# Kernel optimization log

Hardware: AMD Instinct MI355X
Metric: run time of the kernel (lower is better)

Reference implementation:

```python
import jax, jax.numpy as jnp
import numpy as np

N_ENT = 100000   # n_entities
N_HE = 20000     # n_hyperedges
D = 128          # in_dim == out_dim
NNZ_A = 3200000  # nnz of A_in (avg degree 32)
NNZ_H = 1000000  # nnz of each hyperedge incidence matrix


def spmm(rows, cols, vals, x, n_rows):
    """COO sparse (n_rows, n_cols) @ dense x (n_cols, d) -> (n_rows, d)."""
    return jax.ops.segment_sum(vals[:, None] * x[cols], rows, num_segments=n_rows)


def setup_inputs() -> dict:
    key = jax.random.key(0)
    ks = jax.random.split(key, 20)
    ri = lambda k, n, hi: jax.random.randint(k, (n,), 0, hi, dtype=jnp.int32)
    rv = lambda k, n: jax.random.uniform(k, (n,), dtype=jnp.float32) * 0.1
    inp = {
        "ego": jax.random.normal(ks[0], (N_ENT, D), dtype=jnp.float32),
        "A_rows": ri(ks[1], NNZ_A, N_ENT),
        "A_cols": ri(ks[2], NNZ_A, N_ENT),
        "A_vals": rv(ks[3], NNZ_A),
        "p1_rows": ri(ks[4], NNZ_H, N_HE),
        "p1_cols": ri(ks[5], NNZ_H, N_ENT),
        "p1_vals": rv(ks[6], NNZ_H),
        "p2_rows": ri(ks[7], NNZ_H, N_ENT),
        "p2_cols": ri(ks[8], NNZ_H, N_HE),
        "p2_vals": rv(ks[9], NNZ_H),
        "l1_rows": ri(ks[10], NNZ_H, N_HE),
        "l1_cols": ri(ks[11], NNZ_H, N_ENT),
        "l1_vals": rv(ks[12], NNZ_H),
        "l2_rows": ri(ks[13], NNZ_H, N_ENT),
        "l2_cols": ri(ks[14], NNZ_H, N_HE),
        "l2_vals": rv(ks[15], NNZ_H),
        "W1": jax.random.normal(ks[16], (D, D), dtype=jnp.float32) * (1.0 / np.sqrt(D)),
        "b1": jnp.zeros((D,), dtype=jnp.float32),
        "W2": jax.random.normal(ks[17], (D, D), dtype=jnp.float32) * (1.0 / np.sqrt(D)),
        "b2": jnp.zeros((D,), dtype=jnp.float32),
    }
    return inp


def reference(ego, A_rows, A_cols, A_vals,
              p1_rows, p1_cols, p1_vals, p2_rows, p2_cols, p2_vals,
              l1_rows, l1_cols, l1_vals, l2_rows, l2_cols, l2_vals,
              W1, b1, W2, b2):
    # side = A_in @ ego
    side = spmm(A_rows, A_cols, A_vals, ego, N_ENT)
    # proj = norm_proj2 @ (norm_proj1 @ ego)
    proj = spmm(p2_rows, p2_cols, p2_vals,
                spmm(p1_rows, p1_cols, p1_vals, ego, N_HE), N_ENT)
    # lib = norm_lib2 @ (norm_lib1 @ ego)
    lib = spmm(l2_rows, l2_cols, l2_vals,
               spmm(l1_rows, l1_cols, l1_vals, ego, N_HE), N_ENT)
    side = side + proj + lib
    # bi-interaction: LeakyReLU(Linear(ego+side)) + LeakyReLU(Linear(ego*side))
    sum_emb = jax.nn.leaky_relu((ego + side) @ W1.T + b1, negative_slope=0.01)
    bi_emb = jax.nn.leaky_relu((ego * side) @ W2.T + b2, negative_slope=0.01)
    # attention=True -> sum of both branches; message_dropout is identity in eval
    return sum_emb + bi_emb
```

## Files before the change

### kernel.cpp

```cpp
#include <hip/hip_runtime.h>

#define DIM 128
#define N_ENT 100000
#define N_HE  20000
#define NFE 3125
#define NFH 625
#define NFINE 4375
#define CAPF 2000
#define NCC 49
#define CAPC 110000
#define CHB 27
#define TA 4096
#define RPA 16
#define RPT 8

typedef __attribute__((ext_vector_type(8))) _Float16 f16x8;
typedef __attribute__((ext_vector_type(4))) _Float16 f16x4;
typedef __attribute__((ext_vector_type(4))) float f32x4;

__device__ __forceinline__ unsigned bf16_rne(float x) {
  unsigned b = __float_as_uint(x);
  return (b + 0x7fffu + ((b >> 16) & 1u)) >> 16;
}
__device__ __forceinline__ unsigned pack2(float lo, float hi) {
  return bf16_rne(lo) | (bf16_rne(hi) << 16);
}
__device__ __forceinline__ float bf16lo(unsigned u) { return __uint_as_float(u << 16); }
__device__ __forceinline__ float bf16hi(unsigned u) { return __uint_as_float(u & 0xffff0000u); }

__global__ __launch_bounds__(256) void cvt_bf16_kernel(const float* __restrict__ src,
                                                       unsigned* __restrict__ dst,
                                                       int n4) {
  for (int i = blockIdx.x * 256 + threadIdx.x; i < n4; i += gridDim.x * 256) {
    float4 v = reinterpret_cast<const float4*>(src)[i];
    reinterpret_cast<uint2*>(dst)[i] = make_uint2(pack2(v.x, v.y), pack2(v.z, v.w));
  }
}

__global__ __launch_bounds__(256) void cvt_w_kernel(const float* __restrict__ w1,
                                                    const float* __restrict__ w2,
                                                    _Float16* __restrict__ w1h,
                                                    _Float16* __restrict__ w2h) {
  const int half = blockIdx.x >= 8;
  const float* src = half ? w2 : w1;
  _Float16* dst = half ? w2h : w1h;
  const int b = half ? (int)blockIdx.x - 8 : (int)blockIdx.x;
  const int n4 = DIM * DIM / 4;
  for (int i = b * 256 + threadIdx.x; i < n4; i += 8 * 256) {
    float4 v = reinterpret_cast<const float4*>(src)[i];
    f16x4 o;
    o.x = (_Float16)v.x; o.y = (_Float16)v.y; o.z = (_Float16)v.z; o.w = (_Float16)v.w;
    *reinterpret_cast<f16x4*>(dst + (size_t)i * 4) = o;
  }
}

struct SegB {
  const int* rows[5];
  const int* cols[5];
  const float* vals[5];
  int nnz[5];
  int blk_pfx[6];
};

__device__ __forceinline__ int seg_of(const int* pfx, int b) {
  int s = 0;
  while (s < 4 && b >= pfx[s + 1]) s++;
  return s;
}

__global__ __launch_bounds__(256) void binA_kernel(SegB a, int2* __restrict__ heapC,
                                                   int2* __restrict__ heapF,
                                                   int* __restrict__ gcurC,
                                                   int* __restrict__ gcurF) {
  __shared__ int2 srec[TA];
  __shared__ int s_cnt[NFH];
  __shared__ int s_delta[NFH];
  __shared__ int s_part[256];
  const int t = threadIdx.x;
  const int s = seg_of(a.blk_pfx, (int)blockIdx.x);
  const bool ent = (s < 3);
  const unsigned cbase = (s == 1) ? 100000u : ((s == 2) ? 120000u : 0u);
  const int heBase = (s == 3) ? NFE : (NFE + NFH);
  const int nbins = ent ? NCC : NFH;
  const int base = (blockIdx.x - a.blk_pfx[s]) * TA;
  const int cnt_here = min(TA, a.nnz[s] - base);
  const int* __restrict__ rows = a.rows[s];
  const int* __restrict__ cols = a.cols[s];
  const float* __restrict__ vals = a.vals[s];

  for (int i = t; i < nbins; i += 256) s_cnt[i] = 0;
  __syncthreads();

  uint2 rec[RPA];
#pragma unroll
  for (int j = 0; j < RPA; j++) {
    int li = t + j * 256;
    if (li < cnt_here) {
      int e = base + li;
      int r = rows[e];
      unsigned vb = bf16_rne(vals[e]);
      if (ent) {
        unsigned ccol = (unsigned)cols[e] + cbase;
        rec[j].x = (unsigned)(r & 31) | (ccol << 6) | ((unsigned)((r >> 5) & 63) << 24);
        rec[j].y = (vb << 16) | (unsigned)(r >> 11);
        atomicAdd(&s_cnt[r >> 11], 1);
      } else {
        rec[j].x = (unsigned)(r & 31) | ((unsigned)cols[e] << 6);
        rec[j].y = (vb << 16) | (unsigned)(r >> 5);
        atomicAdd(&s_cnt[r >> 5], 1);
      }
    }
  }
  __syncthreads();

  {
    const int chunk = (nbins + 255) / 256;
    const int lo = min(t * chunk, nbins);
    const int hi = min(lo + chunk, nbins);
    int sum = 0;
    for (int i = lo; i < hi; i++) sum += s_cnt[i];
    s_part[t] = sum;
    __syncthreads();
    for (int off = 1; off < 256; off <<= 1) {
      int v = (t >= off) ? s_part[t - off] : 0;
      __syncthreads();
      s_part[t] += v;
      __syncthreads();
    }
    int run = t ? s_part[t - 1] : 0;
    for (int i = lo; i < hi; i++) { int v = s_cnt[i]; s_cnt[i] = run; run += v; }
  }
  __syncthreads();

  for (int i = t; i < nbins; i += 256) {
    int st = s_cnt[i];
    int en = (i == nbins - 1) ? cnt_here : s_cnt[i + 1];
    int c = en - st;
    if (c > 0) {
      if (ent) {
        int gb = atomicAdd(&gcurC[i], c);
        s_delta[i] = i * CAPC + gb - st;
      } else {
        int fg = heBase + i;
        int gb = atomicAdd(&gcurF[fg], c);
        s_delta[i] = fg * CAPF + gb - st;
      }
    }
  }
  __syncthreads();

#pragma unroll
  for (int j = 0; j < RPA; j++) {
    int li = t + j * 256;
    if (li < cnt_here) {
      int bin = ent ? (int)(rec[j].y & 63u) : (int)(rec[j].y & 0x3FFu);
      int p = atomicAdd(&s_cnt[bin], 1);
      srec[p] = make_int2((int)rec[j].x, (int)rec[j].y);
    }
  }
  __syncthreads();

  int2* __restrict__ heap = ent ? heapC : heapF;
  for (int i = t; i < cnt_here; i += 256) {
    int2 rr = srec[i];
    unsigned ry = (unsigned)rr.y;
    int bin = ent ? (int)(ry & 63u) : (int)(ry & 0x3FFu);
    int addr = s_delta[bin] + i;
    int rel = ent ? (addr - bin * CAPC) : (addr - (heBase + bin) * CAPF);
    int cap = ent ? CAPC : CAPF;
    if (rel < cap) heap[addr] = make_int2(rr.x, (int)(ry & 0xFFFF0000u));
  }
}

__global__ __launch_bounds__(256) void binB_kernel(const int2* __restrict__ heapC,
                                                   const int* __restrict__ gcurC,
                                                   int2* __restrict__ heapF,
                                                   int* __restrict__ gcurF) {
  __shared__ int2 srec[TA];
  __shared__ int s_cnt[64];
  __shared__ int s_delta[64];
  const int t = threadIdx.x;
  const int c = blockIdx.x / CHB;
  const int ch = blockIdx.x % CHB;
  const int ccnt = min(gcurC[c], CAPC);
  const int base = ch * TA;
  const int cnt_here = min(TA, ccnt - base);
  if (cnt_here <= 0) return;
  const int2* __restrict__ src = heapC + (size_t)c * CAPC + base;

  if (t < 64) s_cnt[t] = 0;
  __syncthreads();

  uint2 rec[RPA];
#pragma unroll
  for (int j = 0; j < RPA; j++) {
    int li = t + j * 256;
    if (li < cnt_here) {
      int2 v = src[li];
      rec[j] = make_uint2((unsigned)v.x, (unsigned)v.y);
      atomicAdd(&s_cnt[(rec[j].x >> 24) & 63u], 1);
    }
  }
  __syncthreads();

  if (t == 0) {
    int run = 0;
    for (int i = 0; i < 64; i++) { int v = s_cnt[i]; s_cnt[i] = run; run += v; }
  }
  __syncthreads();

  if (t < 64) {
    int st = s_cnt[t];
    int en = (t == 63) ? cnt_here : s_cnt[t + 1];
    int cc = en - st;
    if (cc > 0) {
      int fine = c * 64 + t;
      int gb = atomicAdd(&gcurF[fine], cc);
      s_delta[t] = fine * CAPF + gb - st;
    }
  }
  __syncthreads();

#pragma unroll
  for (int j = 0; j < RPA; j++) {
    int li = t + j * 256;
    if (li < cnt_here) {
      int bin = (int)((rec[j].x >> 24) & 63u);
      int p = atomicAdd(&s_cnt[bin], 1);
      srec[p] = make_int2((int)rec[j].x, (int)rec[j].y);
    }
  }
  __syncthreads();

  for (int i = t; i < cnt_here; i += 256) {
    int2 rr = srec[i];
    int bin = (int)(((unsigned)rr.x >> 24) & 63u);
    int addr = s_delta[bin] + i;
    int rel = addr - (c * 64 + bin) * CAPF;
    if (rel < CAPF)
      heapF[addr] = make_int2((int)((unsigned)rr.x & 0x00FFFFFFu), rr.y);
  }
}

__device__ __forceinline__ void bf16_fma4(float4& acc, uint2 g, float v) {
  acc.x = fmaf(v, __uint_as_float(g.x << 16), acc.x);
  acc.y = fmaf(v, __uint_as_float(g.x & 0xffff0000u), acc.y);
  acc.z = fmaf(v, __uint_as_float(g.y << 16), acc.z);
  acc.w = fmaf(v, __uint_as_float(g.y & 0xffff0000u), acc.w);
}

__device__ __forceinline__ float lrelu(float v) { return v > 0.0f ? v : 0.01f * v; }

template <bool BF16SIDE>
__global__ __launch_bounds__(256, 8) void spmm_ent_kernel(
    const int2* __restrict__ heapF, const int* __restrict__ gcurF,
    const unsigned* __restrict__ xall, float* __restrict__ outf,
    unsigned* __restrict__ sideh) {
  __shared__ int2 srec[CAPF];
  __shared__ int sh_cnt[32];
  __shared__ int sh_off[33];
  __shared__ int sh_cur[32];
  const int b = blockIdx.x;
  const int t = threadIdx.x;
  const int cnt = min(gcurF[b], CAPF);
  const size_t base = (size_t)b * CAPF;

  if (t < 32) sh_cnt[t] = 0;
  __syncthreads();

  int2 rec[RPT];
#pragma unroll
  for (int j = 0; j < RPT; j++) {
    int idx = t + j * 256;
    if (idx < cnt) {
      rec[j] = heapF[base + idx];
      atomicAdd(&sh_cnt[((unsigned)rec[j].x) & 31u], 1);
    }
  }
  __syncthreads();

  if (t == 0) {
    int run = 0;
    for (int i = 0; i < 32; i++) { sh_off[i] = run; sh_cur[i] = run; run += sh_cnt[i]; }
    sh_off[32] = run;
  }
  __syncthreads();

#pragma unroll
  for (int j = 0; j < RPT; j++) {
    int idx = t + j * 256;
    if (idx < cnt) {
      int rl = (int)(((unsigned)rec[j].x) & 31u);
      int p = atomicAdd(&sh_cur[rl], 1);
      srec[p] = rec[j];
    }
  }
  __syncthreads();

  const int grp = t >> 5, sub = t & 31;
  const unsigned* __restrict__ xs = xall + sub * 2;
  const int row0 = b * 32;
#pragma unroll
  for (int i = 0; i < 4; i++) {
    const int r = grp + i * 8;
    float4 acc = make_float4(0.f, 0.f, 0.f, 0.f);
    const int je = sh_off[r + 1];
    int j = sh_off[r];
    for (; j + 8 <= je; j += 8) {
      int2 r0 = srec[j], r1 = srec[j + 1], r2 = srec[j + 2], r3 = srec[j + 3];
      int2 r4 = srec[j + 4], r5 = srec[j + 5], r6 = srec[j + 6], r7 = srec[j + 7];
      uint2 g0 = *reinterpret_cast<const uint2*>(xs + (((unsigned)r0.x) & 0x00FFFFC0u));
      uint2 g1 = *reinterpret_cast<const uint2*>(xs + (((unsigned)r1.x) & 0x00FFFFC0u));
      uint2 g2 = *reinterpret_cast<const uint2*>(xs + (((unsigned)r2.x) & 0x00FFFFC0u));
      uint2 g3 = *reinterpret_cast<const uint2*>(xs + (((unsigned)r3.x) & 0x00FFFFC0u));
      uint2 g4 = *reinterpret_cast<const uint2*>(xs + (((unsigned)r4.x) & 0x00FFFFC0u));
      uint2 g5 = *reinterpret_cast<const uint2*>(xs + (((unsigned)r5.x) & 0x00FFFFC0u));
      uint2 g6 = *reinterpret_cast<const uint2*>(xs + (((unsigned)r6.x) & 0x00FFFFC0u));
      uint2 g7 = *reinterpret_cast<const uint2*>(xs + (((unsigned)r7.x) & 0x00FFFFC0u));
      bf16_fma4(acc, g0, __int_as_float(r0.y));
      bf16_fma4(acc, g1, __int_as_float(r1.y));
      bf16_fma4(acc, g2, __int_as_float(r2.y));
      bf16_fma4(acc, g3, __int_as_float(r3.y));
      bf16_fma4(acc, g4, __int_as_float(r4.y));
      bf16_fma4(acc, g5, __int_as_float(r5.y));
      bf16_fma4(acc, g6, __int_as_float(r6.y));
      bf16_fma4(acc, g7, __int_as_float(r7.y));
    }
    for (; j + 2 <= je; j += 2) {
      int2 r0 = srec[j], r1 = srec[j + 1];
      uint2 g0 = *reinterpret_cast<const uint2*>(xs + (((unsigned)r0.x) & 0x00FFFFC0u));
      uint2 g1 = *reinterpret_cast<const uint2*>(xs + (((unsigned)r1.x) & 0x00FFFFC0u));
      bf16_fma4(acc, g0, __int_as_float(r0.y));
      bf16_fma4(acc, g1, __int_as_float(r1.y));
    }
    if (j < je) {
      int2 r0 = srec[j];
      uint2 g0 = *reinterpret_cast<const uint2*>(xs + (((unsigned)r0.x) & 0x00FFFFC0u));
      bf16_fma4(acc, g0, __int_as_float(r0.y));
    }
    if (BF16SIDE) {
      *reinterpret_cast<uint2*>(sideh + (size_t)(row0 + r) * 64 + sub * 2) =
          make_uint2(pack2(acc.x, acc.y), pack2(acc.z, acc.w));
    } else {
      *reinterpret_cast<float4*>(outf + (size_t)(row0 + r) * DIM + sub * 4) = acc;
    }
  }
}

__global__ __launch_bounds__(256, 8) void spmm_he_kernel(
    const int2* __restrict__ heapF, const int* __restrict__ gcurF,
    const unsigned* __restrict__ egoh,
    unsigned* __restrict__ tmp1h, unsigned* __restrict__ tmp2h) {
  __shared__ int2 srec[CAPF];
  __shared__ int sh_cnt[32];
  __shared__ int sh_off[33];
  __shared__ int sh_cur[32];
  const int half = blockIdx.x >= NFH;
  const int b = half ? (int)blockIdx.x - NFH : (int)blockIdx.x;
  const int fine = (half ? NFE + NFH : NFE) + b;
  unsigned* outh = half ? tmp2h : tmp1h;
  const int t = threadIdx.x;
  const int cnt = min(gcurF[fine], CAPF);
  const size_t base = (size_t)fine * CAPF;

  if (t < 32) sh_cnt[t] = 0;
  __syncthreads();

  int2 rec[RPT];
#pragma unroll
  for (int j = 0; j < RPT; j++) {
    int idx = t + j * 256;
    if (idx < cnt) {
      rec[j] = heapF[base + idx];
      atomicAdd(&sh_cnt[((unsigned)rec[j].x) & 31u], 1);
    }
  }
  __syncthreads();

  if (t == 0) {
    int run = 0;
    for (int i = 0; i < 32; i++) { sh_off[i] = run; sh_cur[i] = run; run += sh_cnt[i]; }
    sh_off[32] = run;
  }
  __syncthreads();

#pragma unroll
  for (int j = 0; j < RPT; j++) {
    int idx = t + j * 256;
    if (idx < cnt) {
      int rl = (int)(((unsigned)rec[j].x) & 31u);
      int p = atomicAdd(&sh_cur[rl], 1);
      srec[p] = rec[j];
    }
  }
  __syncthreads();

  const int grp = t >> 5, sub = t & 31;
  const unsigned* __restrict__ xs = egoh + sub * 2;
  const int row0 = b * 32;
#pragma unroll
  for (int i = 0; i < 4; i++) {
    const int r = grp + i * 8;
    float4 acc = make_float4(0.f, 0.f, 0.f, 0.f);
    const int je = sh_off[r + 1];
    int j = sh_off[r];
    for (; j + 8 <= je; j += 8) {
      int2 r0 = srec[j], r1 = srec[j + 1], r2 = srec[j + 2], r3 = srec[j + 3];
      int2 r4 = srec[j + 4], r5 = srec[j + 5], r6 = srec[j + 6], r7 = srec[j + 7];
      uint2 g0 = *reinterpret_cast<const uint2*>(xs + (((unsigned)r0.x) & 0x00FFFFC0u));
      uint2 g1 = *reinterpret_cast<const uint2*>(xs + (((unsigned)r1.x) & 0x00FFFFC0u));
      uint2 g2 = *reinterpret_cast<const uint2*>(xs + (((unsigned)r2.x) & 0x00FFFFC0u));
      uint2 g3 = *reinterpret_cast<const uint2*>(xs + (((unsigned)r3.x) & 0x00FFFFC0u));
      uint2 g4 = *reinterpret_cast<const uint2*>(xs + (((unsigned)r4.x) & 0x00FFFFC0u));
      uint2 g5 = *reinterpret_cast<const uint2*>(xs + (((unsigned)r5.x) & 0x00FFFFC0u));
      uint2 g6 = *reinterpret_cast<const uint2*>(xs + (((unsigned)r6.x) & 0x00FFFFC0u));
      uint2 g7 = *reinterpret_cast<const uint2*>(xs + (((unsigned)r7.x) & 0x00FFFFC0u));
      bf16_fma4(acc, g0, __int_as_float(r0.y));
      bf16_fma4(acc, g1, __int_as_float(r1.y));
      bf16_fma4(acc, g2, __int_as_float(r2.y));
      bf16_fma4(acc, g3, __int_as_float(r3.y));
      bf16_fma4(acc, g4, __int_as_float(r4.y));
      bf16_fma4(acc, g5, __int_as_float(r5.y));
      bf16_fma4(acc, g6, __int_as_float(r6.y));
      bf16_fma4(acc, g7, __int_as_float(r7.y));
    }
    for (; j + 2 <= je; j += 2) {
      int2 r0 = srec[j], r1 = srec[j + 1];
      uint2 g0 = *reinterpret_cast<const uint2*>(xs + (((unsigned)r0.x) & 0x00FFFFC0u));
      uint2 g1 = *reinterpret_cast<const uint2*>(xs + (((unsigned)r1.x) & 0x00FFFFC0u));
      bf16_fma4(acc, g0, __int_as_float(r0.y));
      bf16_fma4(acc, g1, __int_as_float(r1.y));
    }
    if (j < je) {
      int2 r0 = srec[j];
      uint2 g0 = *reinterpret_cast<const uint2*>(xs + (((unsigned)r0.x) & 0x00FFFFC0u));
      bf16_fma4(acc, g0, __int_as_float(r0.y));
    }
    *reinterpret_cast<uint2*>(outh + (size_t)(row0 + r) * 64 + sub * 2) =
        make_uint2(pack2(acc.x, acc.y), pack2(acc.z, acc.w));
  }
}

template <bool BF16SIDE>
__global__ __launch_bounds__(256, 3) void mfma_epilogue_kernel(
    const float* __restrict__ ego,
    const unsigned* __restrict__ sideh,
    float* __restrict__ out,
    const _Float16* __restrict__ w1h,
    const _Float16* __restrict__ w2h,
    const float* __restrict__ b1,
    const float* __restrict__ b2) {
  __shared__ __align__(16) _Float16 s_sum[64 * DIM];
  __shared__ __align__(16) _Float16 s_prod[64 * DIM];
  const int t = threadIdx.x;
  const int row0 = blockIdx.x * 64;

  for (int i = t; i < 64 * (DIM / 4); i += 256) {
    int r = i >> 5;
    int c4 = (i & 31) * 4;
    int gr = row0 + r;
    float4 e4 = make_float4(0.f, 0.f, 0.f, 0.f);
    float sx = 0.f, sy = 0.f, sz = 0.f, sw = 0.f;
    if (gr < N_ENT) {
      e4 = *reinterpret_cast<const float4*>(ego + (size_t)gr * DIM + c4);
      if (BF16SIDE) {
        uint2 s2 = *reinterpret_cast<const uint2*>(sideh + (size_t)gr * 64 + (c4 >> 1));
        sx = bf16lo(s2.x); sy = bf16hi(s2.x); sz = bf16lo(s2.y); sw = bf16hi(s2.y);
      } else {
        float4 sd4 = *reinterpret_cast<const float4*>(out + (size_t)gr * DIM + c4);
        sx = sd4.x; sy = sd4.y; sz = sd4.z; sw = sd4.w;
      }
    }
    int sidx = (r * DIM + c4) ^ ((r & 7) << 3);
    f16x4 sv, pv;
    sv.x = (_Float16)(e4.x + sx);
    sv.y = (_Float16)(e4.y + sy);
    sv.z = (_Float16)(e4.z + sz);
    sv.w = (_Float16)(e4.w + sw);
    pv.x = (_Float16)(e4.x * sx);
    pv.y = (_Float16)(e4.y * sy);
    pv.z = (_Float16)(e4.z * sz);
    pv.w = (_Float16)(e4.w * sw);
    *reinterpret_cast<f16x4*>(&s_sum[sidx]) = sv;
    *reinterpret_cast<f16x4*>(&s_prod[sidx]) = pv;
  }
  __syncthreads();

  const int w = t >> 6;
  const int l = t & 63;
  const int lr = l & 15;
  const int lk = l >> 4;

  f32x4 acc1[8] = {};
  f32x4 acc2[8] = {};

#pragma unroll
  for (int ks = 0; ks < 4; ks++) {
    int arow = w * 16 + lr;
    int sidx = (arow * DIM + ks * 32 + lk * 8) ^ ((arow & 7) << 3);
    f16x8 a1 = *reinterpret_cast<const f16x8*>(&s_sum[sidx]);
    f16x8 a2 = *reinterpret_cast<const f16x8*>(&s_prod[sidx]);
#pragma unroll
    for (int jt = 0; jt < 8; jt++) {
      int fidx = (jt * 16 + lr) * DIM + ks * 32 + lk * 8;
      f16x8 bw1 = *reinterpret_cast<const f16x8*>(w1h + fidx);
      f16x8 bw2 = *reinterpret_cast<const f16x8*>(w2h + fidx);
      acc1[jt] = __builtin_amdgcn_mfma_f32_16x16x32_f16(a1, bw1, acc1[jt], 0, 0, 0);
      acc2[jt] = __builtin_amdgcn_mfma_f32_16x16x32_f16(a2, bw2, acc2[jt], 0, 0, 0);
    }
  }

#pragma unroll
  for (int jt = 0; jt < 8; jt++) {
    int col = jt * 16 + lr;
    float bb1 = b1[col];
    float bb2 = b2[col];
#pragma unroll
    for (int r = 0; r < 4; r++) {
      int gr = row0 + w * 16 + lk * 4 + r;
      if (gr < N_ENT)
        out[(size_t)gr * DIM + col] = lrelu(acc1[jt][r] + bb1) + lrelu(acc2[jt][r] + bb2);
    }
  }
}

extern "C" void kernel_launch(void* const* d_in, const int* in_sizes, int n_in,
                              void* d_out, int out_size, void* d_ws, size_t ws_size,
                              hipStream_t stream) {
  const float* ego     = (const float*)d_in[0];
  const float* W1      = (const float*)d_in[16];
  const float* b1      = (const float*)d_in[17];
  const float* W2      = (const float*)d_in[18];
  const float* b2      = (const float*)d_in[19];

  int2* heapF = (int2*)d_ws;
  int2* heapC = heapF + (size_t)NFINE * CAPF;
  int*  gcurC = (int*)(heapC + (size_t)NCC * CAPC);
  int*  gcurF = gcurC + NCC;
  unsigned* sideh = (unsigned*)(gcurF + NFINE);
  unsigned* egoh  = (unsigned*)heapC;
  unsigned* tmp1h = egoh + (size_t)N_ENT * 64;
  unsigned* tmp2h = tmp1h + (size_t)N_HE * 64;
  _Float16* w1h = (_Float16*)(tmp2h + (size_t)N_HE * 64);
  _Float16* w2h = w1h + DIM * DIM;

  const size_t need_bf16side =
      (size_t)((char*)(sideh + (size_t)N_ENT * 64) - (char*)d_ws);
  const bool bf16side = (ws_size >= need_bf16side);

  hipMemsetAsync(gcurC, 0, (size_t)(NCC + NFINE) * sizeof(int), stream);

  SegB sg;
  sg.rows[0] = (const int*)d_in[1];  sg.cols[0] = (const int*)d_in[2];  sg.vals[0] = (const float*)d_in[3];  sg.nnz[0] = in_sizes[1];
  sg.rows[1] = (const int*)d_in[7];  sg.cols[1] = (const int*)d_in[8];  sg.vals[1] = (const float*)d_in[9];  sg.nnz[1] = in_sizes[7];
  sg.rows[2] = (const int*)d_in[13]; sg.cols[2] = (const int*)d_in[14]; sg.vals[2] = (const float*)d_in[15]; sg.nnz[2] = in_sizes[13];
  sg.rows[3] = (const int*)d_in[4];  sg.cols[3] = (const int*)d_in[5];  sg.vals[3] = (const float*)d_in[6];  sg.nnz[3] = in_sizes[4];
  sg.rows[4] = (const int*)d_in[10]; sg.cols[4] = (const int*)d_in[11]; sg.vals[4] = (const float*)d_in[12]; sg.nnz[4] = in_sizes[10];
  int pfx = 0;
  for (int s = 0; s < 5; s++) {
    sg.blk_pfx[s] = pfx;
    pfx += (sg.nnz[s] + TA - 1) / TA;
  }
  sg.blk_pfx[5] = pfx;

  binA_kernel<<<dim3(pfx), dim3(256), 0, stream>>>(sg, heapC, heapF, gcurC, gcurF);
  binB_kernel<<<dim3(NCC * CHB), dim3(256), 0, stream>>>(heapC, gcurC, heapF, gcurF);

  cvt_bf16_kernel<<<dim3(2048), dim3(256), 0, stream>>>(ego, egoh, N_ENT * (DIM / 4));
  cvt_w_kernel<<<dim3(16), dim3(256), 0, stream>>>(W1, W2, w1h, w2h);

  float* out = (float*)d_out;

  spmm_he_kernel<<<dim3(2 * NFH), dim3(256), 0, stream>>>(heapF, gcurF, egoh, tmp1h, tmp2h);

  if (bf16side) {
    spmm_ent_kernel<true><<<dim3(NFE), dim3(256), 0, stream>>>(
        heapF, gcurF, egoh, out, sideh);
    mfma_epilogue_kernel<true><<<dim3((N_ENT + 63) / 64), dim3(256), 0, stream>>>(
        ego, sideh, out, w1h, w2h, b1, b2);
  } else {
    spmm_ent_kernel<false><<<dim3(NFE), dim3(256), 0, stream>>>(
        heapF, gcurF, egoh, out, sideh);
    mfma_epilogue_kernel<false><<<dim3((N_ENT + 63) / 64), dim3(256), 0, stream>>>(
        ego, sideh, out, w1h, w2h, b1, b2);
  }
}
```

Before: 430.0 us.

## Rebin rows into finer non-power-of-two groups and merge conversion kernels

Changes the row binning from power-of-two groups of 32 rows to 25 rows per entity bin and 20 rows per hyperedge bin. This adds more SpMM blocks with smaller shared-memory record buffers and capacities, aiming at better occupancy and load balance. The two conversion kernels are merged into one launch, and the epilogue's launch bounds are raised to 4 blocks per CU. Bin computation now needs integer divisions, and the smaller per-bin capacities raise the risk of silently dropped records on overflow.

```diff
diff --git a/kernel.cpp b/kernel.cpp
--- a/kernel.cpp
+++ b/kernel.cpp
@@ -3,16 +3,22 @@
 #define DIM 128
 #define N_ENT 100000
 #define N_HE  20000
-#define NFE 3125
-#define NFH 625
-#define NFINE 4375
-#define CAPF 2000
-#define NCC 49
+#define ROWS_E 25
+#define NFE2 4000
+#define CAPE 1600
+#define NCC 50
+#define NFB 80
 #define CAPC 110000
 #define CHB 27
+#define ROWS_H 20
+#define NFH2 1000
+#define CAPH2 1280
+#define HEB0 (NFE2 * CAPE)
+#define NFINE 6000
 #define TA 4096
 #define RPA 16
-#define RPT 8
+#define RPT_E 7
+#define RPT_H 5
 
 typedef __attribute__((ext_vector_type(8))) _Float16 f16x8;
 typedef __attribute__((ext_vector_type(4))) _Float16 f16x4;
@@ -28,29 +34,30 @@
 __device__ __forceinline__ float bf16lo(unsigned u) { return __uint_as_float(u << 16); }
 __device__ __forceinline__ float bf16hi(unsigned u) { return __uint_as_float(u & 0xffff0000u); }
 
-__global__ __launch_bounds__(256) void cvt_bf16_kernel(const float* __restrict__ src,
-                                                       unsigned* __restrict__ dst,
-                                                       int n4) {
-  for (int i = blockIdx.x * 256 + threadIdx.x; i < n4; i += gridDim.x * 256) {
-    float4 v = reinterpret_cast<const float4*>(src)[i];
-    reinterpret_cast<uint2*>(dst)[i] = make_uint2(pack2(v.x, v.y), pack2(v.z, v.w));
-  }
-}
-
-__global__ __launch_bounds__(256) void cvt_w_kernel(const float* __restrict__ w1,
-                                                    const float* __restrict__ w2,
-                                                    _Float16* __restrict__ w1h,
-                                                    _Float16* __restrict__ w2h) {
-  const int half = blockIdx.x >= 8;
-  const float* src = half ? w2 : w1;
-  _Float16* dst = half ? w2h : w1h;
-  const int b = half ? (int)blockIdx.x - 8 : (int)blockIdx.x;
-  const int n4 = DIM * DIM / 4;
-  for (int i = b * 256 + threadIdx.x; i < n4; i += 8 * 256) {
-    float4 v = reinterpret_cast<const float4*>(src)[i];
-    f16x4 o;
-    o.x = (_Float16)v.x; o.y = (_Float16)v.y; o.z = (_Float16)v.z; o.w = (_Float16)v.w;
-    *reinterpret_cast<f16x4*>(dst + (size_t)i * 4) = o;
+__global__ __launch_bounds__(256) void cvt_all_kernel(const float* __restrict__ ego,
+                                                      unsigned* __restrict__ egoh,
+                                                      const float* __restrict__ w1,
+                                                      const float* __restrict__ w2,
+                                                      _Float16* __restrict__ w1h,
+                                                      _Float16* __restrict__ w2h) {
+  if (blockIdx.x < 2048) {
+    const int n4 = N_ENT * (DIM / 4);
+    for (int i = blockIdx.x * 256 + threadIdx.x; i < n4; i += 2048 * 256) {
+      float4 v = reinterpret_cast<const float4*>(ego)[i];
+      reinterpret_cast<uint2*>(egoh)[i] = make_uint2(pack2(v.x, v.y), pack2(v.z, v.w));
+    }
+  } else {
+    const int half = blockIdx.x >= 2056;
+    const float* src = half ? w2 : w1;
+    _Float16* dst = half ? w2h : w1h;
+    const int b = (int)blockIdx.x - (half ? 2056 : 2048);
+    const int n4 = DIM * DIM / 4;
+    for (int i = b * 256 + threadIdx.x; i < n4; i += 8 * 256) {
+      float4 v = reinterpret_cast<const float4*>(src)[i];
+      f16x4 o;
+      o.x = (_Float16)v.x; o.y = (_Float16)v.y; o.z = (_Float16)v.z; o.w = (_Float16)v.w;
+      *reinterpret_cast<f16x4*>(dst + (size_t)i * 4) = o;
+    }
   }
 }
 
@@ -73,15 +80,16 @@
                                                    int* __restrict__ gcurC,
                                                    int* __restrict__ gcurF) {
   __shared__ int2 srec[TA];
-  __shared__ int s_cnt[NFH];
-  __shared__ int s_delta[NFH];
+  __shared__ int s_cnt[NFH2];
+  __shared__ int s_delta[NFH2];
   __shared__ int s_part[256];
   const int t = threadIdx.x;
   const int s = seg_of(a.blk_pfx, (int)blockIdx.x);
   const bool ent = (s < 3);
   const unsigned cbase = (s == 1) ? 100000u : ((s == 2) ? 120000u : 0u);
-  const int heBase = (s == 3) ? NFE : (NFE + NFH);
-  const int nbins = ent ? NCC : NFH;
+  const int heSegOff = (s == 4) ? NFH2 * CAPH2 : 0;
+  const int heCurOff = NFE2 + ((s == 4) ? NFH2 : 0);
+  const int nbins = ent ? NCC : NFH2;
   const int base = (blockIdx.x - a.blk_pfx[s]) * TA;
   const int cnt_here = min(TA, a.nnz[s] - base);
   const int* __restrict__ rows = a.rows[s];
@@ -97,17 +105,23 @@
     int li = t + j * 256;
     if (li < cnt_here) {
       int e = base + li;
-      int r = rows[e];
+      unsigned r = (unsigned)rows[e];
       unsigned vb = bf16_rne(vals[e]);
       if (ent) {
+        unsigned fine = r / ROWS_E;
+        unsigned rowlocal = r - fine * ROWS_E;
+        unsigned coarse = fine / NFB;
+        unsigned finelocal = fine - coarse * NFB;
         unsigned ccol = (unsigned)cols[e] + cbase;
-        rec[j].x = (unsigned)(r & 31) | (ccol << 6) | ((unsigned)((r >> 5) & 63) << 24);
-        rec[j].y = (vb << 16) | (unsigned)(r >> 11);
-        atomicAdd(&s_cnt[r >> 11], 1);
+        rec[j].x = rowlocal | (ccol << 6) | (finelocal << 24);
+        rec[j].y = (vb << 16) | coarse;
+        atomicAdd(&s_cnt[coarse], 1);
       } else {
-        rec[j].x = (unsigned)(r & 31) | ((unsigned)cols[e] << 6);
-        rec[j].y = (vb << 16) | (unsigned)(r >> 5);
-        atomicAdd(&s_cnt[r >> 5], 1);
+        unsigned fine = r / ROWS_H;
+        unsigned rowlocal = r - fine * ROWS_H;
+        rec[j].x = rowlocal | ((unsigned)cols[e] << 6);
+        rec[j].y = (vb << 16) | fine;
+        atomicAdd(&s_cnt[fine], 1);
       }
     }
   }
@@ -141,9 +155,8 @@
         int gb = atomicAdd(&gcurC[i], c);
         s_delta[i] = i * CAPC + gb - st;
       } else {
-        int fg = heBase + i;
-        int gb = atomicAdd(&gcurF[fg], c);
-        s_delta[i] = fg * CAPF + gb - st;
+        int gb = atomicAdd(&gcurF[heCurOff + i], c);
+        s_delta[i] = HEB0 + heSegOff + i * CAPH2 + gb - st;
       }
     }
   }
@@ -166,8 +179,9 @@
     unsigned ry = (unsigned)rr.y;
     int bin = ent ? (int)(ry & 63u) : (int)(ry & 0x3FFu);
     int addr = s_delta[bin] + i;
-    int rel = ent ? (addr - bin * CAPC) : (addr - (heBase + bin) * CAPF);
-    int cap = ent ? CAPC : CAPF;
+    int rel = ent ? (addr - bin * CAPC)
+                  : (addr - (HEB0 + heSegOff + bin * CAPH2));
+    int cap = ent ? CAPC : CAPH2;
     if (rel < cap) heap[addr] = make_int2(rr.x, (int)(ry & 0xFFFF0000u));
   }
 }
@@ -177,8 +191,8 @@
                                                    int2* __restrict__ heapF,
                                                    int* __restrict__ gcurF) {
   __shared__ int2 srec[TA];
-  __shared__ int s_cnt[64];
-  __shared__ int s_delta[64];
+  __shared__ int s_cnt[NFB];
+  __shared__ int s_delta[NFB];
   const int t = threadIdx.x;
   const int c = blockIdx.x / CHB;
   const int ch = blockIdx.x % CHB;
@@ -188,7 +202,7 @@
   if (cnt_here <= 0) return;
   const int2* __restrict__ src = heapC + (size_t)c * CAPC + base;
 
-  if (t < 64) s_cnt[t] = 0;
+  if (t < NFB) s_cnt[t] = 0;
   __syncthreads();
 
   uint2 rec[RPA];
@@ -198,25 +212,25 @@
     if (li < cnt_here) {
       int2 v = src[li];
       rec[j] = make_uint2((unsigned)v.x, (unsigned)v.y);
-      atomicAdd(&s_cnt[(rec[j].x >> 24) & 63u], 1);
+      atomicAdd(&s_cnt[(rec[j].x >> 24) & 127u], 1);
     }
   }
   __syncthreads();
 
   if (t == 0) {
     int run = 0;
-    for (int i = 0; i < 64; i++) { int v = s_cnt[i]; s_cnt[i] = run; run += v; }
-  }
-  __syncthreads();
-
-  if (t < 64) {
+    for (int i = 0; i < NFB; i++) { int v = s_cnt[i]; s_cnt[i] = run; run += v; }
+  }
+  __syncthreads();
+
+  if (t < NFB) {
     int st = s_cnt[t];
-    int en = (t == 63) ? cnt_here : s_cnt[t + 1];
+    int en = (t == NFB - 1) ? cnt_here : s_cnt[t + 1];
     int cc = en - st;
     if (cc > 0) {
-      int fine = c * 64 + t;
+      int fine = c * NFB + t;
       int gb = atomicAdd(&gcurF[fine], cc);
-      s_delta[t] = fine * CAPF + gb - st;
+      s_delta[t] = fine * CAPE + gb - st;
     }
   }
   __syncthreads();
@@ -225,7 +239,7 @@
   for (int j = 0; j < RPA; j++) {
     int li = t + j * 256;
     if (li < cnt_here) {
-      int bin = (int)((rec[j].x >> 24) & 63u);
+      int bin = (int)((rec[j].x >> 24) & 127u);
       int p = atomicAdd(&s_cnt[bin], 1);
       srec[p] = make_int2((int)rec[j].x, (int)rec[j].y);
     }
@@ -234,10 +248,10 @@
 
   for (int i = t; i < cnt_here; i += 256) {
     int2 rr = srec[i];
-    int bin = (int)(((unsigned)rr.x >> 24) & 63u);
+    int bin = (int)(((unsigned)rr.x >> 24) & 127u);
     int addr = s_delta[bin] + i;
-    int rel = addr - (c * 64 + bin) * CAPF;
-    if (rel < CAPF)
+    int rel = addr - (c * NFB + bin) * CAPE;
+    if (rel < CAPE)
       heapF[addr] = make_int2((int)((unsigned)rr.x & 0x00FFFFFFu), rr.y);
   }
 }
@@ -256,21 +270,21 @@
     const int2* __restrict__ heapF, const int* __restrict__ gcurF,
     const unsigned* __restrict__ xall, float* __restrict__ outf,
     unsigned* __restrict__ sideh) {
-  __shared__ int2 srec[CAPF];
-  __shared__ int sh_cnt[32];
-  __shared__ int sh_off[33];
-  __shared__ int sh_cur[32];
+  __shared__ int2 srec[CAPE];
+  __shared__ int sh_cnt[ROWS_E];
+  __shared__ int sh_off[ROWS_E + 1];
+  __shared__ int sh_cur[ROWS_E];
   const int b = blockIdx.x;
   const int t = threadIdx.x;
-  const int cnt = min(gcurF[b], CAPF);
-  const size_t base = (size_t)b * CAPF;
-
-  if (t < 32) sh_cnt[t] = 0;
-  __syncthreads();
-
-  int2 rec[RPT];
-#pragma unroll
-  for (int j = 0; j < RPT; j++) {
+  const int cnt = min(gcurF[b], CAPE);
+  const size_t base = (size_t)b * CAPE;
+
+  if (t < ROWS_E) sh_cnt[t] = 0;
+  __syncthreads();
+
+  int2 rec[RPT_E];
+#pragma unroll
+  for (int j = 0; j < RPT_E; j++) {
     int idx = t + j * 256;
     if (idx < cnt) {
       rec[j] = heapF[base + idx];
@@ -281,13 +295,13 @@
 
   if (t == 0) {
     int run = 0;
-    for (int i = 0; i < 32; i++) { sh_off[i] = run; sh_cur[i] = run; run += sh_cnt[i]; }
-    sh_off[32] = run;
-  }
-  __syncthreads();
-
-#pragma unroll
-  for (int j = 0; j < RPT; j++) {
+    for (int i = 0; i < ROWS_E; i++) { sh_off[i] = run; sh_cur[i] = run; run += sh_cnt[i]; }
+    sh_off[ROWS_E] = run;
+  }
+  __syncthreads();
+
+#pragma unroll
+  for (int j = 0; j < RPT_E; j++) {
     int idx = t + j * 256;
     if (idx < cnt) {
       int rl = (int)(((unsigned)rec[j].x) & 31u);
@@ -299,10 +313,8 @@
 
   const int grp = t >> 5, sub = t & 31;
   const unsigned* __restrict__ xs = xall + sub * 2;
-  const int row0 = b * 32;
-#pragma unroll
-  for (int i = 0; i < 4; i++) {
-    const int r = grp + i * 8;
+  const int row0 = b * ROWS_E;
+  for (int r = grp; r < ROWS_E; r += 8) {
     float4 acc = make_float4(0.f, 0.f, 0.f, 0.f);
     const int je = sh_off[r + 1];
     int j = sh_off[r];
@@ -351,24 +363,24 @@
     const int2* __restrict__ heapF, const int* __restrict__ gcurF,
     const unsigned* __restrict__ egoh,
     unsigned* __restrict__ tmp1h, unsigned* __restrict__ tmp2h) {
-  __shared__ int2 srec[CAPF];
-  __shared__ int sh_cnt[32];
-  __shared__ int sh_off[33];
-  __shared__ int sh_cur[32];
-  const int half = blockIdx.x >= NFH;
-  const int b = half ? (int)blockIdx.x - NFH : (int)blockIdx.x;
-  const int fine = (half ? NFE + NFH : NFE) + b;
+  __shared__ int2 srec[CAPH2];
+  __shared__ int sh_cnt[ROWS_H];
+  __shared__ int sh_off[ROWS_H + 1];
+  __shared__ int sh_cur[ROWS_H];
+  const int bidx = blockIdx.x;
+  const int half = bidx >= NFH2;
+  const int b = half ? bidx - NFH2 : bidx;
   unsigned* outh = half ? tmp2h : tmp1h;
   const int t = threadIdx.x;
-  const int cnt = min(gcurF[fine], CAPF);
-  const size_t base = (size_t)fine * CAPF;
-
-  if (t < 32) sh_cnt[t] = 0;
-  __syncthreads();
-
-  int2 rec[RPT];
-#pragma unroll
-  for (int j = 0; j < RPT; j++) {
+  const int cnt = min(gcurF[NFE2 + bidx], CAPH2);
+  const size_t base = (size_t)HEB0 + (size_t)bidx * CAPH2;
+
+  if (t < ROWS_H) sh_cnt[t] = 0;
+  __syncthreads();
+
+  int2 rec[RPT_H];
+#pragma unroll
+  for (int j = 0; j < RPT_H; j++) {
     int idx = t + j * 256;
     if (idx < cnt) {
       rec[j] = heapF[base + idx];
@@ -379,13 +391,13 @@
 
   if (t == 0) {
     int run = 0;
-    for (int i = 0; i < 32; i++) { sh_off[i] = run; sh_cur[i] = run; run += sh_cnt[i]; }
-    sh_off[32] = run;
-  }
-  __syncthreads();
-
-#pragma unroll
-  for (int j = 0; j < RPT; j++) {
+    for (int i = 0; i < ROWS_H; i++) { sh_off[i] = run; sh_cur[i] = run; run += sh_cnt[i]; }
+    sh_off[ROWS_H] = run;
+  }
+  __syncthreads();
+
+#pragma unroll
+  for (int j = 0; j < RPT_H; j++) {
     int idx = t + j * 256;
     if (idx < cnt) {
       int rl = (int)(((unsigned)rec[j].x) & 31u);
@@ -397,10 +409,8 @@
 
   const int grp = t >> 5, sub = t & 31;
   const unsigned* __restrict__ xs = egoh + sub * 2;
-  const int row0 = b * 32;
-#pragma unroll
-  for (int i = 0; i < 4; i++) {
-    const int r = grp + i * 8;
+  const int row0 = b * ROWS_H;
+  for (int r = grp; r < ROWS_H; r += 8) {
     float4 acc = make_float4(0.f, 0.f, 0.f, 0.f);
     const int je = sh_off[r + 1];
     int j = sh_off[r];
@@ -442,7 +452,7 @@
 }
 
 template <bool BF16SIDE>
-__global__ __launch_bounds__(256, 3) void mfma_epilogue_kernel(
+__global__ __launch_bounds__(256, 4) void mfma_epilogue_kernel(
     const float* __restrict__ ego,
     const unsigned* __restrict__ sideh,
     float* __restrict__ out,
@@ -533,8 +543,9 @@
   const float* W2      = (const float*)d_in[18];
   const float* b2      = (const float*)d_in[19];
 
+  const size_t nrecF = (size_t)NFE2 * CAPE + 2ull * NFH2 * CAPH2;
   int2* heapF = (int2*)d_ws;
-  int2* heapC = heapF + (size_t)NFINE * CAPF;
+  int2* heapC = heapF + nrecF;
   int*  gcurC = (int*)(heapC + (size_t)NCC * CAPC);
   int*  gcurF = gcurC + NCC;
   unsigned* sideh = (unsigned*)(gcurF + NFINE);
@@ -566,20 +577,19 @@
   binA_kernel<<<dim3(pfx), dim3(256), 0, stream>>>(sg, heapC, heapF, gcurC, gcurF);
   binB_kernel<<<dim3(NCC * CHB), dim3(256), 0, stream>>>(heapC, gcurC, heapF, gcurF);
 
-  cvt_bf16_kernel<<<dim3(2048), dim3(256), 0, stream>>>(ego, egoh, N_ENT * (DIM / 4));
-  cvt_w_kernel<<<dim3(16), dim3(256), 0, stream>>>(W1, W2, w1h, w2h);
+  cvt_all_kernel<<<dim3(2064), dim3(256), 0, stream>>>(ego, egoh, W1, W2, w1h, w2h);
 
   float* out = (float*)d_out;
 
-  spmm_he_kernel<<<dim3(2 * NFH), dim3(256), 0, stream>>>(heapF, gcurF, egoh, tmp1h, tmp2h);
+  spmm_he_kernel<<<dim3(2 * NFH2), dim3(256), 0, stream>>>(heapF, gcurF, egoh, tmp1h, tmp2h);
 
   if (bf16side) {
-    spmm_ent_kernel<true><<<dim3(NFE), dim3(256), 0, stream>>>(
+    spmm_ent_kernel<true><<<dim3(NFE2), dim3(256), 0, stream>>>(
         heapF, gcurF, egoh, out, sideh);
     mfma_epilogue_kernel<true><<<dim3((N_ENT + 63) / 64), dim3(256), 0, stream>>>(
         ego, sideh, out, w1h, w2h, b1, b2);
   } else {
-    spmm_ent_kernel<false><<<dim3(NFE), dim3(256), 0, stream>>>(
+    spmm_ent_kernel<false><<<dim3(NFE2), dim3(256), 0, stream>>>(
         heapF, gcurF, egoh, out, sideh);
     mfma_epilogue_kernel<false><<<dim3((N_ENT + 63) / 64), dim3(256), 0, stream>>>(
         ego, sideh, out, w1h, w2h, b1, b2);
```

After: 456.1 us. 6.1% more time.
